# Kernel optimization log

Measured on AMD Instinct MI355X. Metric: run time of the kernel, lower is better.

The kernel has to match this reference:

```python
import jax, jax.numpy as jnp
import numpy as np

EPS = 1e-10

def setup_inputs() -> dict:
    key = jax.random.key(0)
    ks = jax.random.split(key, 7)
    B, S, C, H, W = 8, 4, 512, 64, 64
    Cq = C // 4
    x = jax.random.normal(ks[0], (B, S, C, H, W), dtype=jnp.float32)
    wq = jax.random.normal(ks[1], (S, Cq, C), dtype=jnp.float32) * 0.02
    bq = jax.random.normal(ks[2], (S, Cq), dtype=jnp.float32) * 0.02
    wk = jax.random.normal(ks[3], (S, Cq, C), dtype=jnp.float32) * 0.02
    bk = jax.random.normal(ks[4], (S, Cq), dtype=jnp.float32) * 0.02
    wv = jax.random.normal(ks[5], (S, C, C), dtype=jnp.float32) * 0.02
    bv = jax.random.normal(ks[6], (S, C), dtype=jnp.float32) * 0.02
    gamma = jnp.zeros((1,), dtype=jnp.float32)
    return {"x": x, "wq": wq, "bq": bq, "wk": wk, "bk": bk,
            "wv": wv, "bv": bv, "gamma": gamma}

def reference(x, wq, bq, wk, bk, wv, bv, gamma):
    # x: (B, S, C, H, W); per-scale 1x1 convs == per-pixel matmuls
    B, S, C, H, W = x.shape
    q = jnp.einsum('bschw,soc->bsohw', x, wq) + bq[None, :, :, None, None]
    k = jnp.einsum('bschw,soc->bsohw', x, wk) + bk[None, :, :, None, None]
    v = jnp.einsum('bschw,soc->bsohw', x, wv) + bv[None, :, :, None, None]
    pq = q.reshape(B, S, -1)                      # (B, S, D)
    pk = k.reshape(B, S, -1).transpose(0, 2, 1)   # (B, D, S)
    pv = v.reshape(B, S, -1)                      # (B, S, C*H*W)
    # L2 normalization (cosine similarity), matching torch eps placement
    A1 = pq / (jnp.sqrt(jnp.sum(pq * pq, axis=-1, keepdims=True)) + EPS)
    B1 = pk / (jnp.sqrt(jnp.sum(pk * pk, axis=1, keepdims=True)) + EPS)
    energy = jnp.einsum('bsd,bdt->bst', A1, B1)   # (B, S, S)
    attention = jax.nn.softmax(energy, axis=-1)
    out = jnp.einsum('bst,btd->bsd', attention, pv).reshape(B, S, C, H, W)
    out = gamma[0] * out + x
    # original returns list [out[:, i]] for i in range(S); return stacked tensor
    return out
```

## Files before the change

### kernel.cpp

```cpp
#include <hip/hip_runtime.h>
#include <hip/hip_bf16.h>

#define EPS_F 1e-10f

typedef short s16x8 __attribute__((ext_vector_type(8)));
typedef float f32x4 __attribute__((ext_vector_type(4)));
typedef unsigned short ushort_t;

constexpr int B_ = 8, S_ = 4, C_ = 512, Cq_ = 128, HW_ = 4096;
constexpr long long D_ = (long long)Cq_ * HW_;

__device__ inline float bf_lo(unsigned int u) { return __uint_as_float(u << 16); }
__device__ inline float bf_hi(unsigned int u) { return __uint_as_float(u & 0xffff0000u); }

__device__ inline ushort_t f2bf(float f) {
    __hip_bfloat16 h = __float2bfloat16(f);
    return *reinterpret_cast<ushort_t*>(&h);
}
__device__ inline unsigned int pack_bf2(float a, float b) {
    return (unsigned int)f2bf(a) | ((unsigned int)f2bf(b) << 16);
}
__device__ inline float dot8(uint4 a, uint4 b) {
    return bf_lo(a.x) * bf_lo(b.x) + bf_hi(a.x) * bf_hi(b.x)
         + bf_lo(a.y) * bf_lo(b.y) + bf_hi(a.y) * bf_hi(b.y)
         + bf_lo(a.z) * bf_lo(b.z) + bf_hi(a.z) * bf_hi(b.z)
         + bf_lo(a.w) * bf_lo(b.w) + bf_hi(a.w) * bf_hi(b.w);
}

#define GLOAD16(gp, lp) __builtin_amdgcn_global_load_lds( \
    (const __attribute__((address_space(1))) unsigned int*)(gp), \
    (__attribute__((address_space(3))) unsigned int*)(lp), 16, 0, 0)

#define VMCNT(n) asm volatile("s_waitcnt vmcnt(" #n ")" ::: "memory")
#define VMCNT0 asm volatile("s_waitcnt vmcnt(0)" ::: "memory")
#define LGK0   asm volatile("s_waitcnt lgkmcnt(0)" ::: "memory")
#define MFMA16(a, b, c) __builtin_amdgcn_mfma_f32_16x16x32_bf16(a, b, c, 0, 0, 0)

#define SWZ(p) ((((p) >> 3) & 7) ^ ((p) & 7))

__global__ __launch_bounds__(256) void prep3(
    const float* __restrict__ wq, const float* __restrict__ wk,
    const float* __restrict__ wv,
    ushort_t* __restrict__ Wqk_pre, ushort_t* __restrict__ Wvb_pre,
    float* __restrict__ g4) {
    int gid = blockIdx.x * 256 + threadIdx.x;
    if (gid < 8 * 24 * 16) g4[gid] = 0.f;
    if (gid < 65536) {
        int s = gid >> 14;
        int kt = (gid >> 11) & 7;
        int row = (gid >> 3) & 255;
        int slot = gid & 7;
        int col = kt * 64 + ((slot ^ (row & 7)) << 3);
        const float* src = (row < 128)
            ? &wq[((size_t)s * 128 + row) * 512 + col]
            : &wk[((size_t)s * 128 + (row - 128)) * 512 + col];
        float4 f0 = *reinterpret_cast<const float4*>(src);
        float4 f1 = *reinterpret_cast<const float4*>(src + 4);
        uint4 o;
        o.x = pack_bf2(f0.x, f0.y); o.y = pack_bf2(f0.z, f0.w);
        o.z = pack_bf2(f1.x, f1.y); o.w = pack_bf2(f1.z, f1.w);
        *reinterpret_cast<uint4*>(Wqk_pre + (size_t)gid * 8) = o;
    } else {
        int c2 = gid - 65536;
        int t = c2 >> 15;
        int ct = (c2 >> 14) & 1;
        int kt = (c2 >> 11) & 7;
        int row = (c2 >> 3) & 255;
        int slot = c2 & 7;
        int col = kt * 64 + ((slot ^ (row & 7)) << 3);
        const float* src = &wv[((size_t)t * 512 + ct * 256 + row) * 512 + col];
        float4 f0 = *reinterpret_cast<const float4*>(src);
        float4 f1 = *reinterpret_cast<const float4*>(src + 4);
        uint4 o;
        o.x = pack_bf2(f0.x, f0.y); o.y = pack_bf2(f0.z, f0.w);
        o.z = pack_bf2(f1.x, f1.y); o.w = pack_bf2(f1.z, f1.w);
        *reinterpret_cast<uint4*>(Wvb_pre + (size_t)c2 * 8) = o;
    }
}

__global__ __launch_bounds__(512, 8) void qk8(
    const ushort_t* __restrict__ Wqk_pre, const float* __restrict__ x,
    const float* __restrict__ bq, const float* __restrict__ bk,
    ushort_t* __restrict__ Qb, ushort_t* __restrict__ Kb,
    ushort_t* __restrict__ xbfT) {

    const int xcd = blockIdx.x & 7;
    const int idx = blockIdx.x >> 3;
    const int bt = xcd * 4 + (idx >> 8);
    const int s = bt & 3;
    const int pb = (idx >> 1) & 127;
    const int ob = idx & 1;
    const int p0 = pb * 32;

    __shared__ __align__(16) ushort_t AsAll[2 * 8192];
    __shared__ __align__(16) ushort_t BsAll[2 * 2048];

    const int tid = threadIdx.x;
    const int w = tid >> 6, lane = tid & 63;
    const int wr = w >> 1, wc = w & 1;
    const int li = lane & 15, lk = lane >> 4;
    const int arow = wr * 32;
    const int bp = wc * 16 + li;
    int a_sl[2], b_sl[2];
#pragma unroll
    for (int h = 0; h < 2; ++h) {
        a_sl[h] = (((h * 4 + lk) ^ (li & 7)) << 3);
        b_sl[h] = (((h * 4 + lk) ^ SWZ(bp)) << 3);
    }

    const int sk = tid >> 3, spb = (tid & 7) * 4;
    const int ep = tid >> 3, esl = tid & 7;
    const int ec = esl ^ SWZ(ep);

    const float* Bx = x + (size_t)bt * C_ * HW_ + p0 + spb;

    f32x4 acc[2];
    acc[0] = 0.f; acc[1] = 0.f;
    float4 nb;

#define STAGE_A8(T, BUF)                                                     \
    { const ushort_t* _tp = Wqk_pre + ((size_t)(s * 8 + (T)) << 14)          \
                            + (ob << 13);                                    \
      ushort_t* _ld = &AsAll[(BUF) * 8192];                                  \
      _Pragma("unroll")                                                      \
      for (int _i = 0; _i < 2; ++_i)                                         \
          GLOAD16(_tp + ((w * 2 + _i) << 9) + (lane << 3),                   \
                  _ld + ((w * 2 + _i) << 9)); }

#define LOAD_B8(T) nb = *reinterpret_cast<const float4*>(Bx + (size_t)((T) * 64 + sk) * HW_)

#define WRITE_B8(BUF)                                                        \
    { float _vv[4] = {nb.x, nb.y, nb.z, nb.w};                               \
      _Pragma("unroll")                                                      \
      for (int _j = 0; _j < 4; ++_j) {                                       \
          int _p = spb + _j;                                                 \
          BsAll[(BUF) * 2048 + _p * 64 + (((sk >> 3) ^ SWZ(_p)) << 3)        \
                + (sk & 7)] = f2bf(_vv[_j]);                                 \
      } }

#define EMIT8(T, BUF)                                                        \
    if (ob == 0 && w < 4) {                                                  \
        s16x8 _ev = *reinterpret_cast<const s16x8*>(&BsAll[(BUF) * 2048 + tid * 8]); \
        *reinterpret_cast<s16x8*>(                                           \
            xbfT + ((size_t)bt * HW_ + p0 + ep) * 512 + (T) * 64 + ec * 8) = _ev; \
    }

#define COMPUTE8(BUF)                                                        \
    { const int _ab = (BUF) * 8192, _bb = (BUF) * 2048;                      \
      _Pragma("unroll")                                                      \
      for (int h = 0; h < 2; ++h) {                                          \
          s16x8 af0 = *reinterpret_cast<const s16x8*>(                       \
              &AsAll[_ab + (arow + 0 * 16 + li) * 64 + a_sl[h]]);            \
          s16x8 af1 = *reinterpret_cast<const s16x8*>(                       \
              &AsAll[_ab + (arow + 1 * 16 + li) * 64 + a_sl[h]]);            \
          s16x8 bf = *reinterpret_cast<const s16x8*>(                        \
              &BsAll[_bb + bp * 64 + b_sl[h]]);                              \
          __builtin_amdgcn_s_setprio(1);                                     \
          acc[0] = MFMA16(af0, bf, acc[0]);                                  \
          acc[1] = MFMA16(af1, bf, acc[1]);                                  \
          __builtin_amdgcn_s_setprio(0);                                     \
      } }

    LOAD_B8(0);
    STAGE_A8(0, 0);
    WRITE_B8(0);
    VMCNT0; LGK0;
    __builtin_amdgcn_s_barrier();

#pragma unroll
    for (int t = 0; t < 8; ++t) {
        if (t < 7) { LOAD_B8(t + 1); STAGE_A8(t + 1, (t + 1) & 1); }
        EMIT8(t, t & 1);
        COMPUTE8(t & 1);
        if (t < 7) {
            WRITE_B8((t + 1) & 1);
            VMCNT0; LGK0;
            __builtin_amdgcn_s_barrier();
        }
    }

#undef STAGE_A8
#undef LOAD_B8
#undef WRITE_B8
#undef EMIT8
#undef COMPUTE8

    ushort_t* outp = ob ? Kb : Qb;
    const float* biasp = ob ? (bk + s * 128) : (bq + s * 128);
#pragma unroll
    for (int mf = 0; mf < 2; ++mf) {
#pragma unroll
        for (int r = 0; r < 4; ++r) {
            int m = arow + mf * 16 + lk * 4 + r;
            float vv = acc[mf][r] + biasp[m];
            int p = p0 + wc * 16 + li;
            outp[(size_t)bt * D_ + (size_t)m * HW_ + p] = f2bf(vv);
        }
    }
}

__global__ __launch_bounds__(256, 4) void vblend9(
    const ushort_t* __restrict__ Wvb_pre, const ushort_t* __restrict__ xbfT,
    const float* __restrict__ x, const float* __restrict__ bv,
    const float* __restrict__ att, const float* __restrict__ gamma,
    float* __restrict__ out) {

    const int b = blockIdx.x & 7;
    const int idx = blockIdx.x >> 3;
    const int cblk = idx & 7;
    const int p0 = (idx >> 3) * 64;
    const int ct = cblk >> 2;
    const int csub = cblk & 3;

    __shared__ __align__(16) ushort_t AsAll[3 * 4096];
    __shared__ __align__(16) ushort_t BsAll[3 * 4096];

    const int tid = threadIdx.x;
    const int w = tid >> 6, lane = tid & 63;
    const int wr2 = w >> 1, wc2 = w & 1;
    const int li = lane & 15, lk = lane >> 4;

    int a_sl[2], b_sl[2];
    const int bp = wc2 * 32 + li;
    const int bp1 = bp + 16;
    int b_sl1[2];
#pragma unroll
    for (int h = 0; h < 2; ++h) {
        a_sl[h] = (((h * 4 + lk) ^ (li & 7)) << 3);
        b_sl[h] = (((h * 4 + lk) ^ SWZ(bp)) << 3);
        b_sl1[h] = (((h * 4 + lk) ^ SWZ(bp1)) << 3);
    }

    float attv[16];
#pragma unroll
    for (int i = 0; i < 16; ++i)
        attv[i] = __uint_as_float(__builtin_amdgcn_readfirstlane(
            __float_as_uint(att[b * 16 + i])));

    const int bst_p0 = tid >> 3, bst_sl0 = tid & 7;
    const int bst_c0 = bst_sl0 ^ SWZ(bst_p0);
    const int bst_p1 = (tid + 256) >> 3, bst_sl1 = tid & 7;
    const int bst_c1 = bst_sl1 ^ SWZ(bst_p1);

    f32x4 acc[2][2];
    f32x4 mst[4][2][2];
#pragma unroll
    for (int mf = 0; mf < 2; ++mf)
#pragma unroll
        for (int nf = 0; nf < 2; ++nf) acc[mf][nf] = 0.f;
#pragma unroll
    for (int so = 0; so < 4; ++so)
#pragma unroll
        for (int mf = 0; mf < 2; ++mf)
#pragma unroll
            for (int nf = 0; nf < 2; ++nf) mst[so][mf][nf] = 0.f;

#define STAGE9(TS, BUF)                                                      \
    {   const int _t = (TS) >> 3, _kt = (TS) & 7;                            \
        const ushort_t* _ap = Wvb_pre +                                      \
            (((size_t)(_t * 2 + ct) * 8 + _kt) << 14) + (csub << 12);        \
        ushort_t* _al = &AsAll[(BUF) * 4096];                                \
        GLOAD16(_ap + (size_t)(w << 9) + (size_t)(lane << 3),                \
                _al + (w << 9));                                             \
        GLOAD16(_ap + 2048 + (size_t)(w << 9) + (size_t)(lane << 3),         \
                _al + 2048 + (w << 9));                                      \
        const ushort_t* _bb = xbfT + ((size_t)(b * 4 + _t) * HW_);           \
        GLOAD16(_bb + ((size_t)(p0 + bst_p0)) * 512 + _kt * 64 + bst_c0 * 8, \
                &BsAll[(BUF) * 4096 + (w << 9)]);                            \
        GLOAD16(_bb + ((size_t)(p0 + bst_p1)) * 512 + _kt * 64 + bst_c1 * 8, \
                &BsAll[(BUF) * 4096 + 2048 + (w << 9)]);                     \
    }

#define COMPUTE9(BUF)                                                       \
    {   const int _ab = (BUF) * 4096, _bbf = (BUF) * 4096;                  \
        _Pragma("unroll")                                                    \
        for (int h = 0; h < 2; ++h) {                                        \
            s16x8 af0 = *reinterpret_cast<const s16x8*>(                     \
                &AsAll[_ab + (wr2 * 32 + 0 * 16 + li) * 64 + a_sl[h]]);      \
            s16x8 af1 = *reinterpret_cast<const s16x8*>(                     \
                &AsAll[_ab + (wr2 * 32 + 1 * 16 + li) * 64 + a_sl[h]]);      \
            s16x8 bf0 = *reinterpret_cast<const s16x8*>(                     \
                &BsAll[_bbf + bp * 64 + b_sl[h]]);                           \
            s16x8 bf1 = *reinterpret_cast<const s16x8*>(                     \
                &BsAll[_bbf + bp1 * 64 + b_sl1[h]]);                         \
            __builtin_amdgcn_s_setprio(1);                                   \
            acc[0][0] = MFMA16(af0, bf0, acc[0][0]);                         \
            acc[0][1] = MFMA16(af0, bf1, acc[0][1]);                         \
            acc[1][0] = MFMA16(af1, bf0, acc[1][0]);                         \
            acc[1][1] = MFMA16(af1, bf1, acc[1][1]);                         \
            __builtin_amdgcn_s_setprio(0);                                   \
        } }

#define BLEND9(T2)                                                           \
    { _Pragma("unroll")                                                      \
      for (int _so = 0; _so < 4; ++_so)                                      \
          _Pragma("unroll")                                                  \
          for (int _mf = 0; _mf < 2; ++_mf)                                  \
              _Pragma("unroll")                                              \
              for (int _nf = 0; _nf < 2; ++_nf)                              \
                  mst[_so][_mf][_nf] += attv[_so * 4 + (T2)] * acc[_mf][_nf];\
      _Pragma("unroll")                                                      \
      for (int _mf = 0; _mf < 2; ++_mf)                                      \
          _Pragma("unroll")                                                  \
          for (int _nf = 0; _nf < 2; ++_nf) acc[_mf][_nf] = 0.f; }

    STAGE9(0, 0);
    STAGE9(1, 1);
    VMCNT(4);
    __builtin_amdgcn_s_barrier();

#pragma unroll
    for (int ts = 0; ts < 32; ++ts) {
        if (ts + 2 < 32) STAGE9(ts + 2, (ts + 2) % 3);
        COMPUTE9(ts % 3);
        if (ts == 7)  BLEND9(0);
        if (ts == 15) BLEND9(1);
        if (ts == 23) BLEND9(2);
        if (ts == 31) BLEND9(3);
        if (ts < 31) {
            if (ts + 2 < 32) { VMCNT(4); } else { VMCNT0; }
            __builtin_amdgcn_s_barrier();
        }
    }

#undef STAGE9
#undef COMPUTE9
#undef BLEND9

    const float gm = gamma[0];
    const int c0 = cblk * 64;
#pragma unroll
    for (int mf = 0; mf < 2; ++mf) {
#pragma unroll
        for (int r = 0; r < 4; ++r) {
            int c = c0 + wr2 * 32 + mf * 16 + lk * 4 + r;
            float bvv[4];
#pragma unroll
            for (int t = 0; t < 4; ++t) bvv[t] = bv[(size_t)t * 512 + c];
#pragma unroll
            for (int so = 0; so < 4; ++so) {
                float bsum = attv[so * 4 + 0] * bvv[0] + attv[so * 4 + 1] * bvv[1]
                           + attv[so * 4 + 2] * bvv[2] + attv[so * 4 + 3] * bvv[3];
#pragma unroll
                for (int nf = 0; nf < 2; ++nf) {
                    int p = p0 + wc2 * 32 + nf * 16 + li;
                    size_t off = ((size_t)(b * 4 + so) * C_ + c) * HW_ + p;
                    out[off] = gm * (mst[so][mf][nf][r] + bsum) + x[off];
                }
            }
        }
    }
}

__global__ __launch_bounds__(256) void gram5(
    const ushort_t* __restrict__ Q, const ushort_t* __restrict__ K,
    float* __restrict__ g4) {

    const int ch = blockIdx.x;
    const int b  = blockIdx.y;
    const size_t base = (size_t)ch * (D_ / 16);

    const uint4* qv[4];
    const uint4* kv[4];
#pragma unroll
    for (int s = 0; s < 4; ++s) {
        qv[s] = reinterpret_cast<const uint4*>(Q + (size_t)(b * 4 + s) * D_ + base);
        kv[s] = reinterpret_cast<const uint4*>(K + (size_t)(b * 4 + s) * D_ + base);
    }

    float accr[24];
#pragma unroll
    for (int e = 0; e < 24; ++e) accr[e] = 0.f;

    const int n8 = (int)(D_ / 16 / 8);
    for (int i = threadIdx.x; i < n8; i += 256) {
        uint4 qa[4], ka[4];
#pragma unroll
        for (int s = 0; s < 4; ++s) { qa[s] = qv[s][i]; ka[s] = kv[s][i]; }
#pragma unroll
        for (int s = 0; s < 4; ++s) {
#pragma unroll
            for (int u = 0; u < 4; ++u) accr[s * 4 + u] += dot8(qa[s], ka[u]);
            accr[16 + s] += dot8(qa[s], qa[s]);
            accr[20 + s] += dot8(ka[s], ka[s]);
        }
    }

    __shared__ float red[4][24];
    const int lane = threadIdx.x & 63, wid = threadIdx.x >> 6;
#pragma unroll
    for (int e = 0; e < 24; ++e) {
        float v = accr[e];
#pragma unroll
        for (int o = 32; o > 0; o >>= 1) v += __shfl_down(v, o);
        if (lane == 0) red[wid][e] = v;
    }
    __syncthreads();
    if (threadIdx.x < 24) {
        float t = red[0][threadIdx.x] + red[1][threadIdx.x]
                + red[2][threadIdx.x] + red[3][threadIdx.x];
        g4[((size_t)b * 24 + threadIdx.x) * 16 + ch] = t;
    }
}

__global__ void att_k5(const float* __restrict__ g4, float* __restrict__ att) {
    const int b = threadIdx.x;
    if (b >= B_) return;
    float e_[24];
#pragma unroll
    for (int e = 0; e < 24; ++e) {
        const float* p = g4 + ((size_t)b * 24 + e) * 16;
        float t = 0.f;
#pragma unroll
        for (int ch = 0; ch < 16; ++ch) t += p[ch];
        e_[e] = t;
    }
    float nq[4], nk[4];
#pragma unroll
    for (int s = 0; s < 4; ++s) {
        nq[s] = sqrtf(e_[16 + s]) + EPS_F;
        nk[s] = sqrtf(e_[20 + s]) + EPS_F;
    }
#pragma unroll
    for (int s = 0; s < 4; ++s) {
        float e[4], m = -1e30f;
#pragma unroll
        for (int t = 0; t < 4; ++t) {
            e[t] = e_[s * 4 + t] / (nq[s] * nk[t]);
            m = fmaxf(m, e[t]);
        }
        float sum = 0.f;
#pragma unroll
        for (int t = 0; t < 4; ++t) { e[t] = expf(e[t] - m); sum += e[t]; }
#pragma unroll
        for (int t = 0; t < 4; ++t) att[(size_t)(b * 4 + s) * 4 + t] = e[t] / sum;
    }
}

extern "C" void kernel_launch(void* const* d_in, const int* in_sizes, int n_in,
                              void* d_out, int out_size, void* d_ws, size_t ws_size,
                              hipStream_t stream) {
    const float* x     = (const float*)d_in[0];
    const float* wq    = (const float*)d_in[1];
    const float* bq    = (const float*)d_in[2];
    const float* wk    = (const float*)d_in[3];
    const float* bk    = (const float*)d_in[4];
    const float* wv    = (const float*)d_in[5];
    const float* bv    = (const float*)d_in[6];
    const float* gamma = (const float*)d_in[7];
    float* out = (float*)d_out;

    char* ws = (char*)d_ws;
    const size_t qk_elems = (size_t)B_ * S_ * Cq_ * HW_;
    ushort_t* Qb      = (ushort_t*)ws;
    ushort_t* Kb      = Qb + qk_elems;
    ushort_t* Wqk_pre = Kb + qk_elems;
    ushort_t* Wvb_pre = Wqk_pre + (size_t)4 * 8 * 256 * 64;
    float*    g4      = (float*)(Wvb_pre + (size_t)4 * 2 * 8 * 256 * 64);
    float*    att     = g4 + 8 * 24 * 16;
    ushort_t* xbfT    = (ushort_t*)(att + 128);

    prep3<<<768, 256, 0, stream>>>(wq, wk, wv, Wqk_pre, Wvb_pre, g4);
    qk8<<<8192, 512, 0, stream>>>(Wqk_pre, x, bq, bk, Qb, Kb, xbfT);
    gram5<<<dim3(16, 8), 256, 0, stream>>>(Qb, Kb, g4);
    att_k5<<<1, 64, 0, stream>>>(g4, att);
    vblend9<<<4096, 256, 0, stream>>>(Wvb_pre, xbfT, x, bv, att, gamma, out);
}
```

Before: 408.9 us.

## Store bf16 x in MFMA-fragment layout and load B operands directly to registers

The qk kernel now writes the bf16 copy of x in a layout where each 64-lane wave's MFMA B fragment is contiguous. The vblend kernel then loads its B operands straight from global memory into registers, skipping the LDS staging and its shared buffer. It double-buffers these register fragments across even and odd steps. This removes LDS traffic and shared memory use for B, at the cost of more VGPRs and global loads that now sit directly on the MFMA critical path, with vmcnt accounting that must stay correct.

```diff
diff --git a/kernel.cpp b/kernel.cpp
--- a/kernel.cpp
+++ b/kernel.cpp
@@ -78,11 +78,11 @@
     }
 }
 
-__global__ __launch_bounds__(512, 8) void qk8(
+__global__ __launch_bounds__(512, 8) void qk8f(
     const ushort_t* __restrict__ Wqk_pre, const float* __restrict__ x,
     const float* __restrict__ bq, const float* __restrict__ bk,
     ushort_t* __restrict__ Qb, ushort_t* __restrict__ Kb,
-    ushort_t* __restrict__ xbfT) {
+    ushort_t* __restrict__ xbfF) {
 
     const int xcd = blockIdx.x & 7;
     const int idx = blockIdx.x >> 3;
@@ -109,8 +109,9 @@
     }
 
     const int sk = tid >> 3, spb = (tid & 7) * 4;
-    const int ep = tid >> 3, esl = tid & 7;
-    const int ec = esl ^ SWZ(ep);
+    const int eft = tid >> 6;
+    const int epl = ((eft >> 1) << 4) | li;
+    const int ekc = ((eft & 1) << 2) | lk;
 
     const float* Bx = x + (size_t)bt * C_ * HW_ + p0 + spb;
 
@@ -138,11 +139,13 @@
                 + (sk & 7)] = f2bf(_vv[_j]);                                 \
       } }
 
-#define EMIT8(T, BUF)                                                        \
+#define EMIT8F(T, BUF)                                                       \
     if (ob == 0 && w < 4) {                                                  \
-        s16x8 _ev = *reinterpret_cast<const s16x8*>(&BsAll[(BUF) * 2048 + tid * 8]); \
+        s16x8 _ev = *reinterpret_cast<const s16x8*>(                         \
+            &BsAll[(BUF) * 2048 + epl * 64 + ((ekc ^ SWZ(epl)) << 3)]);      \
         *reinterpret_cast<s16x8*>(                                           \
-            xbfT + ((size_t)bt * HW_ + p0 + ep) * 512 + (T) * 64 + ec * 8) = _ev; \
+            xbfF + (((((size_t)bt * 256) + (p0 >> 4) + (eft >> 1)) * 16      \
+                     + (T) * 2 + (eft & 1)) << 9) + lane * 8) = _ev;         \
     }
 
 #define COMPUTE8(BUF)                                                        \
@@ -170,7 +173,7 @@
 #pragma unroll
     for (int t = 0; t < 8; ++t) {
         if (t < 7) { LOAD_B8(t + 1); STAGE_A8(t + 1, (t + 1) & 1); }
-        EMIT8(t, t & 1);
+        EMIT8F(t, t & 1);
         COMPUTE8(t & 1);
         if (t < 7) {
             WRITE_B8((t + 1) & 1);
@@ -182,7 +185,7 @@
 #undef STAGE_A8
 #undef LOAD_B8
 #undef WRITE_B8
-#undef EMIT8
+#undef EMIT8F
 #undef COMPUTE8
 
     ushort_t* outp = ob ? Kb : Qb;
@@ -199,8 +202,8 @@
     }
 }
 
-__global__ __launch_bounds__(256, 4) void vblend9(
-    const ushort_t* __restrict__ Wvb_pre, const ushort_t* __restrict__ xbfT,
+__global__ __launch_bounds__(256, 4) void vblend10(
+    const ushort_t* __restrict__ Wvb_pre, const ushort_t* __restrict__ xbfF,
     const float* __restrict__ x, const float* __restrict__ bv,
     const float* __restrict__ att, const float* __restrict__ gamma,
     float* __restrict__ out) {
@@ -208,28 +211,22 @@
     const int b = blockIdx.x & 7;
     const int idx = blockIdx.x >> 3;
     const int cblk = idx & 7;
-    const int p0 = (idx >> 3) * 64;
+    const int pblk = idx >> 3;
+    const int p0 = pblk * 64;
     const int ct = cblk >> 2;
     const int csub = cblk & 3;
 
     __shared__ __align__(16) ushort_t AsAll[3 * 4096];
-    __shared__ __align__(16) ushort_t BsAll[3 * 4096];
 
     const int tid = threadIdx.x;
     const int w = tid >> 6, lane = tid & 63;
     const int wr2 = w >> 1, wc2 = w & 1;
     const int li = lane & 15, lk = lane >> 4;
 
-    int a_sl[2], b_sl[2];
-    const int bp = wc2 * 32 + li;
-    const int bp1 = bp + 16;
-    int b_sl1[2];
-#pragma unroll
-    for (int h = 0; h < 2; ++h) {
+    int a_sl[2];
+#pragma unroll
+    for (int h = 0; h < 2; ++h)
         a_sl[h] = (((h * 4 + lk) ^ (li & 7)) << 3);
-        b_sl[h] = (((h * 4 + lk) ^ SWZ(bp)) << 3);
-        b_sl1[h] = (((h * 4 + lk) ^ SWZ(bp1)) << 3);
-    }
 
     float attv[16];
 #pragma unroll
@@ -237,11 +234,6 @@
         attv[i] = __uint_as_float(__builtin_amdgcn_readfirstlane(
             __float_as_uint(att[b * 16 + i])));
 
-    const int bst_p0 = tid >> 3, bst_sl0 = tid & 7;
-    const int bst_c0 = bst_sl0 ^ SWZ(bst_p0);
-    const int bst_p1 = (tid + 256) >> 3, bst_sl1 = tid & 7;
-    const int bst_c1 = bst_sl1 ^ SWZ(bst_p1);
-
     f32x4 acc[2][2];
     f32x4 mst[4][2][2];
 #pragma unroll
@@ -255,43 +247,45 @@
 #pragma unroll
             for (int nf = 0; nf < 2; ++nf) mst[so][mf][nf] = 0.f;
 
-#define STAGE9(TS, BUF)                                                      \
+    s16x8 bE[4], bO[4];
+
+#define STAGE_A10(TS, BUF)                                                   \
     {   const int _t = (TS) >> 3, _kt = (TS) & 7;                            \
         const ushort_t* _ap = Wvb_pre +                                      \
             (((size_t)(_t * 2 + ct) * 8 + _kt) << 14) + (csub << 12);        \
         ushort_t* _al = &AsAll[(BUF) * 4096];                                \
-        GLOAD16(_ap + (size_t)(w << 9) + (size_t)(lane << 3),                \
-                _al + (w << 9));                                             \
-        GLOAD16(_ap + 2048 + (size_t)(w << 9) + (size_t)(lane << 3),         \
-                _al + 2048 + (w << 9));                                      \
-        const ushort_t* _bb = xbfT + ((size_t)(b * 4 + _t) * HW_);           \
-        GLOAD16(_bb + ((size_t)(p0 + bst_p0)) * 512 + _kt * 64 + bst_c0 * 8, \
-                &BsAll[(BUF) * 4096 + (w << 9)]);                            \
-        GLOAD16(_bb + ((size_t)(p0 + bst_p1)) * 512 + _kt * 64 + bst_c1 * 8, \
-                &BsAll[(BUF) * 4096 + 2048 + (w << 9)]);                     \
-    }
-
-#define COMPUTE9(BUF)                                                       \
-    {   const int _ab = (BUF) * 4096, _bbf = (BUF) * 4096;                  \
+        GLOAD16(_ap + (w << 9) + (lane << 3), _al + (w << 9));               \
+        GLOAD16(_ap + 2048 + (w << 9) + (lane << 3), _al + 2048 + (w << 9)); \
+    }
+
+#define LOADB10(TS, DST)                                                     \
+    {   const size_t _fb = (((size_t)(b * 4 + ((TS) >> 3)) * 256             \
+                            + pblk * 4 + wc2 * 2) * 16 + ((TS) & 7) * 2);    \
+        _Pragma("unroll")                                                    \
+        for (int _h = 0; _h < 2; ++_h)                                       \
+            _Pragma("unroll")                                                \
+            for (int _nf = 0; _nf < 2; ++_nf)                                \
+                DST[_h * 2 + _nf] = *reinterpret_cast<const s16x8*>(         \
+                    xbfF + ((_fb + _nf * 16 + _h) << 9) + lane * 8);         \
+    }
+
+#define COMPUTE10(BUF, SRC)                                                  \
+    {   const int _ab = (BUF) * 4096;                                        \
         _Pragma("unroll")                                                    \
         for (int h = 0; h < 2; ++h) {                                        \
             s16x8 af0 = *reinterpret_cast<const s16x8*>(                     \
                 &AsAll[_ab + (wr2 * 32 + 0 * 16 + li) * 64 + a_sl[h]]);      \
             s16x8 af1 = *reinterpret_cast<const s16x8*>(                     \
                 &AsAll[_ab + (wr2 * 32 + 1 * 16 + li) * 64 + a_sl[h]]);      \
-            s16x8 bf0 = *reinterpret_cast<const s16x8*>(                     \
-                &BsAll[_bbf + bp * 64 + b_sl[h]]);                           \
-            s16x8 bf1 = *reinterpret_cast<const s16x8*>(                     \
-                &BsAll[_bbf + bp1 * 64 + b_sl1[h]]);                         \
             __builtin_amdgcn_s_setprio(1);                                   \
-            acc[0][0] = MFMA16(af0, bf0, acc[0][0]);                         \
-            acc[0][1] = MFMA16(af0, bf1, acc[0][1]);                         \
-            acc[1][0] = MFMA16(af1, bf0, acc[1][0]);                         \
-            acc[1][1] = MFMA16(af1, bf1, acc[1][1]);                         \
+            acc[0][0] = MFMA16(af0, SRC[h * 2 + 0], acc[0][0]);              \
+            acc[0][1] = MFMA16(af0, SRC[h * 2 + 1], acc[0][1]);              \
+            acc[1][0] = MFMA16(af1, SRC[h * 2 + 0], acc[1][0]);              \
+            acc[1][1] = MFMA16(af1, SRC[h * 2 + 1], acc[1][1]);              \
             __builtin_amdgcn_s_setprio(0);                                   \
         } }
 
-#define BLEND9(T2)                                                           \
+#define BLEND10(T2)                                                          \
     { _Pragma("unroll")                                                      \
       for (int _so = 0; _so < 4; ++_so)                                      \
           _Pragma("unroll")                                                  \
@@ -304,28 +298,36 @@
           _Pragma("unroll")                                                  \
           for (int _nf = 0; _nf < 2; ++_nf) acc[_mf][_nf] = 0.f; }
 
-    STAGE9(0, 0);
-    STAGE9(1, 1);
-    VMCNT(4);
+    STAGE_A10(0, 0);
+    STAGE_A10(1, 1);
+    LOADB10(0, bE);
+    VMCNT(6);
     __builtin_amdgcn_s_barrier();
 
 #pragma unroll
-    for (int ts = 0; ts < 32; ++ts) {
-        if (ts + 2 < 32) STAGE9(ts + 2, (ts + 2) % 3);
-        COMPUTE9(ts % 3);
-        if (ts == 7)  BLEND9(0);
-        if (ts == 15) BLEND9(1);
-        if (ts == 23) BLEND9(2);
-        if (ts == 31) BLEND9(3);
-        if (ts < 31) {
-            if (ts + 2 < 32) { VMCNT(4); } else { VMCNT0; }
+    for (int ts = 0; ts < 32; ts += 2) {
+        if (ts + 2 < 32) STAGE_A10(ts + 2, (ts + 2) % 3);
+        LOADB10(ts + 1, bO);
+        COMPUTE10(ts % 3, bE);
+        if (ts < 30) { VMCNT(6); } else { VMCNT(4); }
+        __builtin_amdgcn_s_barrier();
+        if (ts + 3 < 32) STAGE_A10(ts + 3, (ts + 3) % 3);
+        if (ts + 2 < 32) LOADB10(ts + 2, bE);
+        COMPUTE10((ts + 1) % 3, bO);
+        if (ts + 1 == 7)  BLEND10(0);
+        if (ts + 1 == 15) BLEND10(1);
+        if (ts + 1 == 23) BLEND10(2);
+        if (ts + 1 == 31) BLEND10(3);
+        if (ts + 1 < 31) {
+            VMCNT(6);
             __builtin_amdgcn_s_barrier();
         }
     }
 
-#undef STAGE9
-#undef COMPUTE9
-#undef BLEND9
+#undef STAGE_A10
+#undef LOADB10
+#undef COMPUTE10
+#undef BLEND10
 
     const float gm = gamma[0];
     const int c0 = cblk * 64;
@@ -458,11 +460,11 @@
     ushort_t* Wvb_pre = Wqk_pre + (size_t)4 * 8 * 256 * 64;
     float*    g4      = (float*)(Wvb_pre + (size_t)4 * 2 * 8 * 256 * 64);
     float*    att     = g4 + 8 * 24 * 16;
-    ushort_t* xbfT    = (ushort_t*)(att + 128);
+    ushort_t* xbfF    = (ushort_t*)(att + 128);
 
     prep3<<<768, 256, 0, stream>>>(wq, wk, wv, Wqk_pre, Wvb_pre, g4);
-    qk8<<<8192, 512, 0, stream>>>(Wqk_pre, x, bq, bk, Qb, Kb, xbfT);
+    qk8f<<<8192, 512, 0, stream>>>(Wqk_pre, x, bq, bk, Qb, Kb, xbfF);
     gram5<<<dim3(16, 8), 256, 0, stream>>>(Qb, Kb, g4);
     att_k5<<<1, 64, 0, stream>>>(g4, att);
-    vblend9<<<4096, 256, 0, stream>>>(Wvb_pre, xbfT, x, bv, att, gamma, out);
-}
+    vblend10<<<4096, 256, 0, stream>>>(Wvb_pre, xbfF, x, bv, att, gamma, out);
+}
```

New measurement: 436.1 us. +6.6%, slower.
